# Optimization experiments

Measured on AMD Instinct MI355X. Metric: run time of the kernel, lower is better.

Reference implementation:

```python
import jax, jax.numpy as jnp
import numpy as np

EMBED_DIM = 1024
NUM_HEADS = 16
HEAD_DIM = EMBED_DIM // NUM_HEADS
LN_EPS = 1e-5


def setup_inputs() -> dict:
    key = jax.random.key(0)
    ks = jax.random.split(key, 10)
    B, S, D = 1, 4096, EMBED_DIM
    s = 1.0 / np.sqrt(D)
    inp = {
        'input': jax.random.normal(ks[0], (B, S, D), dtype=jnp.float32),
        'Wq': jax.random.normal(ks[1], (D, D), dtype=jnp.float32) * s,
        'bq': jnp.zeros((D,), dtype=jnp.float32),
        'Wk': jax.random.normal(ks[2], (D, D), dtype=jnp.float32) * s,
        'bk': jnp.zeros((D,), dtype=jnp.float32),
        'Wv': jax.random.normal(ks[3], (D, D), dtype=jnp.float32) * s,
        'bv': jnp.zeros((D,), dtype=jnp.float32),
        'Wo': jax.random.normal(ks[4], (D, D), dtype=jnp.float32) * s,
        'bo': jnp.zeros((D,), dtype=jnp.float32),
        'ln_gamma': jnp.ones((D,), dtype=jnp.float32),
        'ln_beta': jnp.zeros((D,), dtype=jnp.float32),
    }
    return inp


def reference(input, Wq, bq, Wk, bk, Wv, bv, Wo, bo, ln_gamma, ln_beta):
    B, S, D = input.shape
    H, Hd = NUM_HEADS, HEAD_DIM
    # projections (torch Linear: x @ W.T + b)
    q = input @ Wq.T + bq
    k = input @ Wk.T + bk
    v = input @ Wv.T + bv
    # [B, H, S, Hd]
    q = q.reshape(B, S, H, Hd).transpose(0, 2, 1, 3)
    k = k.reshape(B, S, H, Hd).transpose(0, 2, 1, 3)
    v = v.reshape(B, S, H, Hd).transpose(0, 2, 1, 3)
    scores = jnp.einsum('bhqd,bhkd->bhqk', q, k) / jnp.sqrt(jnp.float32(Hd))
    causal = jnp.tril(jnp.ones((S, S), dtype=bool))  # [S, S]
    scores = jnp.where(causal[None, None, :, :], scores, -jnp.inf)
    attn = jax.nn.softmax(scores, axis=-1)  # stable (max-subtract) internally
    out = jnp.einsum('bhqk,bhkd->bhqd', attn, v)
    out = out.transpose(0, 2, 1, 3).reshape(B, S, D)
    out = out @ Wo.T + bo
    out = out + input
    # LayerNorm
    mu = jnp.mean(out, axis=-1, keepdims=True)
    var = jnp.var(out, axis=-1, keepdims=True)
    normed = (out - mu) * jax.lax.rsqrt(var + LN_EPS)
    return normed * ln_gamma + ln_beta
```

## Files before the change

### kernel.cpp

```cpp
#include <hip/hip_runtime.h>
#include <hip/hip_bf16.h>

typedef float floatx4 __attribute__((ext_vector_type(4)));
typedef short short8 __attribute__((ext_vector_type(8)));

#define S_LEN 4096
#define D_DIM 1024
#define NHEAD 16
#define SCALE_LOG2 0.1803368801111204f

__device__ __forceinline__ void gload_lds16(const void* g, void* l) {
  __builtin_amdgcn_global_load_lds(
      (const __attribute__((address_space(1))) unsigned int*)g,
      (__attribute__((address_space(3))) unsigned int*)l, 16, 0, 0);
}

__device__ __forceinline__ unsigned short f2bf_bits(float f) {
  __hip_bfloat16 h = __float2bfloat16(f);
  return __builtin_bit_cast(unsigned short, h);
}

__global__ __launch_bounds__(256) void cvt_all(const float* __restrict__ x,
                                               const float* __restrict__ w0,
                                               const float* __restrict__ w1,
                                               const float* __restrict__ w2,
                                               const float* __restrict__ w3,
                                               unsigned short* __restrict__ xo,
                                               unsigned short* __restrict__ o0,
                                               unsigned short* __restrict__ o1,
                                               unsigned short* __restrict__ o2,
                                               unsigned short* __restrict__ o3) {
  const int bid = blockIdx.x;
  const float* in;
  unsigned short* out;
  int i;
  if (bid < 4096) {
    in = x;
    out = xo;
    i = bid * 256 + threadIdx.x;
  } else {
    const int which = (bid - 4096) >> 10;
    in = which == 0 ? w0 : which == 1 ? w1 : which == 2 ? w2 : w3;
    out = which == 0 ? o0 : which == 1 ? o1 : which == 2 ? o2 : o3;
    i = ((bid - 4096) & 1023) * 256 + threadIdx.x;
  }
  float4 v = reinterpret_cast<const float4*>(in)[i];
  ushort4 u;
  u.x = f2bf_bits(v.x);
  u.y = f2bf_bits(v.y);
  u.z = f2bf_bits(v.z);
  u.w = f2bf_bits(v.w);
  reinterpret_cast<ushort4*>(out)[i] = u;
}

__global__ __launch_bounds__(256) void gemm_qkv(const unsigned short* __restrict__ A,
                                                const unsigned short* __restrict__ WqB,
                                                const unsigned short* __restrict__ WkB,
                                                const unsigned short* __restrict__ WvB,
                                                const float* __restrict__ bq,
                                                const float* __restrict__ bk,
                                                const float* __restrict__ bv,
                                                unsigned short* __restrict__ Qo,
                                                unsigned short* __restrict__ Ko,
                                                unsigned short* __restrict__ VTo) {
  __shared__ __align__(16) unsigned short As[128 * 32];
  __shared__ __align__(16) unsigned short Bs[128 * 32];
  const int K = 1024, N = 1024, M = 4096;
  const int tid = threadIdx.x;
  const int wave = tid >> 6, lane = tid & 63;
  const int seg = blockIdx.y >> 3;
  const int m0 = blockIdx.x * 128, n0 = (blockIdx.y & 7) * 128;
  const unsigned short* B = seg == 0 ? WqB : seg == 1 ? WkB : WvB;
  const float* bias = seg == 0 ? bq : seg == 1 ? bk : bv;
  const int wr = wave >> 1, wc = wave & 1;

  floatx4 acc[4][4] = {};
  const unsigned short* Ab = A + (size_t)m0 * K;
  const unsigned short* Bb = B + (size_t)n0 * K;
  const int srow = lane >> 2, scol = (lane & 3) * 8;
  const int aRow = lane & 15, kOff = (lane >> 4) * 8;

  for (int k0 = 0; k0 < K; k0 += 32) {
#pragma unroll
    for (int i = 0; i < 2; ++i) {
      const int c = wave * 2 + i;
      const int row = c * 16 + srow;
      gload_lds16(Ab + (size_t)row * K + k0 + scol, &As[c * 512]);
      gload_lds16(Bb + (size_t)row * K + k0 + scol, &Bs[c * 512]);
    }
    __syncthreads();
    short8 af[4], bfg[4];
#pragma unroll
    for (int f = 0; f < 4; ++f) {
      af[f] = *reinterpret_cast<const short8*>(&As[(wr * 64 + f * 16 + aRow) * 32 + kOff]);
      bfg[f] = *reinterpret_cast<const short8*>(&Bs[(wc * 64 + f * 16 + aRow) * 32 + kOff]);
    }
#pragma unroll
    for (int fm = 0; fm < 4; ++fm)
#pragma unroll
      for (int fn = 0; fn < 4; ++fn)
        acc[fm][fn] =
            __builtin_amdgcn_mfma_f32_16x16x32_bf16(af[fm], bfg[fn], acc[fm][fn], 0, 0, 0);
    __syncthreads();
  }

  const int rb = (lane >> 4) * 4, cl = lane & 15;
  const float osc = seg == 0 ? SCALE_LOG2 : 1.0f;
#pragma unroll
  for (int fm = 0; fm < 4; ++fm)
#pragma unroll
    for (int fn = 0; fn < 4; ++fn)
#pragma unroll
      for (int r = 0; r < 4; ++r) {
        const int row = m0 + wr * 64 + fm * 16 + rb + r;
        const int col = n0 + wc * 64 + fn * 16 + cl;
        const float v = (acc[fm][fn][r] + bias[col]) * osc;
        if (seg == 0)
          Qo[(size_t)row * N + col] = f2bf_bits(v);
        else if (seg == 1)
          Ko[(size_t)row * N + col] = f2bf_bits(v);
        else
          VTo[(size_t)col * M + row] = f2bf_bits(v);
      }
}

__global__ __launch_bounds__(256) void gemm_o(const unsigned short* __restrict__ A,
                                              const unsigned short* __restrict__ B,
                                              const float* __restrict__ bias,
                                              const float* __restrict__ resid,
                                              float* __restrict__ C) {
  __shared__ __align__(16) unsigned short As[64 * 32];
  __shared__ __align__(16) unsigned short Bs[128 * 32];
  const int K = 1024, N = 1024;
  const int tid = threadIdx.x;
  const int wave = tid >> 6, lane = tid & 63;
  const int m0 = blockIdx.x * 64, n0 = blockIdx.y * 128;
  const int wr = wave >> 1, wc = wave & 1;

  floatx4 acc[2][4] = {};
  const unsigned short* Ab = A + (size_t)m0 * K;
  const unsigned short* Bb = B + (size_t)n0 * K;
  const int srow = lane >> 2, scol = (lane & 3) * 8;
  const int aRow = lane & 15, kOff = (lane >> 4) * 8;

  for (int k0 = 0; k0 < K; k0 += 32) {
#pragma unroll
    for (int i = 0; i < 3; ++i) {
      const int ci = wave * 3 + i;
      if (ci < 4) {
        const int row = ci * 16 + srow;
        gload_lds16(Ab + (size_t)row * K + k0 + scol, &As[ci * 512]);
      } else {
        const int row = (ci - 4) * 16 + srow;
        gload_lds16(Bb + (size_t)row * K + k0 + scol, &Bs[(ci - 4) * 512]);
      }
    }
    __syncthreads();
    short8 af[2], bfg[4];
#pragma unroll
    for (int f = 0; f < 2; ++f)
      af[f] = *reinterpret_cast<const short8*>(&As[(wr * 32 + f * 16 + aRow) * 32 + kOff]);
#pragma unroll
    for (int f = 0; f < 4; ++f)
      bfg[f] = *reinterpret_cast<const short8*>(&Bs[(wc * 64 + f * 16 + aRow) * 32 + kOff]);
#pragma unroll
    for (int fm = 0; fm < 2; ++fm)
#pragma unroll
      for (int fn = 0; fn < 4; ++fn)
        acc[fm][fn] =
            __builtin_amdgcn_mfma_f32_16x16x32_bf16(af[fm], bfg[fn], acc[fm][fn], 0, 0, 0);
    __syncthreads();
  }

  const int rb = (lane >> 4) * 4, cl = lane & 15;
#pragma unroll
  for (int fm = 0; fm < 2; ++fm)
#pragma unroll
    for (int fn = 0; fn < 4; ++fn)
#pragma unroll
      for (int r = 0; r < 4; ++r) {
        const int row = m0 + wr * 32 + fm * 16 + rb + r;
        const int col = n0 + wc * 64 + fn * 16 + cl;
        C[(size_t)row * N + col] =
            acc[fm][fn][r] + bias[col] + resid[(size_t)row * N + col];
      }
}

__global__ __launch_bounds__(256) void attn_fwd(const unsigned short* __restrict__ Q,
                                                const unsigned short* __restrict__ Kg,
                                                const unsigned short* __restrict__ VT,
                                                unsigned short* __restrict__ O) {
  __shared__ __align__(16) unsigned short Ks[2 * 64 * 64];
  __shared__ __align__(16) unsigned short Vs[2 * 64 * 64];
  __shared__ __align__(16) unsigned short Ps[4][16 * 64];

  const int bid = blockIdx.x;
  const int h = bid & 15;
  const int qt = 63 - (bid >> 4);
  const int q0 = qt * 64;
  const int wave = threadIdx.x >> 6, lane = threadIdx.x & 63;
  const int l15 = lane & 15, l4 = lane >> 4;
  const int q7 = l15 & 7;

  const int qrow = q0 + wave * 16 + l15;
  short8 qf[2];
#pragma unroll
  for (int ks = 0; ks < 2; ++ks)
    qf[ks] = *reinterpret_cast<const short8*>(
        &Q[(size_t)qrow * D_DIM + h * 64 + ks * 32 + l4 * 8]);

  floatx4 acco[4] = {};
  float l_run = 0.f;

  auto stageK = [&](int buf, int t) {
    const int kv0 = t * 64;
#pragma unroll
    for (int i = 0; i < 2; ++i) {
      const int seg = wave * 2 + i;
      const int c = seg * 64 + lane;
      const int r = c >> 3, jj = c & 7;
      const int sj = (jj ^ (r & 7)) * 8;
      gload_lds16(&Kg[(size_t)(kv0 + r) * D_DIM + h * 64 + sj],
                  &Ks[buf * 4096 + seg * 512]);
    }
  };
  auto stageV = [&](int buf, int t) {
    const int kv0 = t * 64;
#pragma unroll
    for (int i = 0; i < 2; ++i) {
      const int seg = wave * 2 + i;
      const int c = seg * 64 + lane;
      const int r = c >> 3, jj = c & 7;
      const int sj = (jj ^ (r & 7)) * 8;
      gload_lds16(&VT[(size_t)(h * 64 + r) * S_LEN + kv0 + sj],
                  &Vs[buf * 4096 + seg * 512]);
    }
  };

  const int ntiles = qt + 1;
  stageK(0, 0);

  for (int t = 0; t < ntiles; ++t) {
    asm volatile("s_waitcnt vmcnt(0)" ::: "memory");
    __builtin_amdgcn_s_barrier();
    if (t + 1 < ntiles) stageK((t + 1) & 1, t + 1);
    stageV(t & 1, t);

    const unsigned short* ksb = &Ks[(t & 1) * 4096];

    floatx4 accs[4] = {};
#pragma unroll
    for (int ks = 0; ks < 2; ++ks)
#pragma unroll
      for (int fn = 0; fn < 4; ++fn) {
        const int R = fn * 16 + l15;
        const int J = ks * 4 + l4;
        const short8 kf =
            *reinterpret_cast<const short8*>(&ksb[R * 64 + ((J ^ (R & 7)) * 8)]);
        accs[fn] =
            __builtin_amdgcn_mfma_f32_16x16x32_bf16(kf, qf[ks], accs[fn], 0, 0, 0);
      }

    if (t > 0) {
      const unsigned short* vsb = &Vs[((t - 1) & 1) * 4096];
#pragma unroll
      for (int kh = 0; kh < 2; ++kh) {
        const short8 pf = *reinterpret_cast<const short8*>(
            &Ps[wave][l15 * 64 + (((kh * 4 + l4) ^ q7) << 3)]);
#pragma unroll
        for (int fn = 0; fn < 4; ++fn) {
          const int R = fn * 16 + l15;
          const int J = kh * 4 + l4;
          const short8 vf =
              *reinterpret_cast<const short8*>(&vsb[R * 64 + ((J ^ (R & 7)) * 8)]);
          acco[fn] = __builtin_amdgcn_mfma_f32_16x16x32_bf16(vf, pf, acco[fn], 0, 0, 0);
        }
      }
    }

    const int kv0 = t * 64;
    float p[4][4];
    if (t == ntiles - 1) {
#pragma unroll
      for (int fn = 0; fn < 4; ++fn)
#pragma unroll
        for (int r = 0; r < 4; ++r) {
          const int ka = kv0 + fn * 16 + l4 * 4 + r;
          const float s = (ka > qrow) ? -1e30f : accs[fn][r];
          p[fn][r] = __builtin_amdgcn_exp2f(s);
        }
    } else {
#pragma unroll
      for (int fn = 0; fn < 4; ++fn)
#pragma unroll
        for (int r = 0; r < 4; ++r) p[fn][r] = __builtin_amdgcn_exp2f(accs[fn][r]);
    }
    float rs = 0.f;
#pragma unroll
    for (int fn = 0; fn < 4; ++fn)
#pragma unroll
      for (int r = 0; r < 4; ++r) rs += p[fn][r];
    l_run += rs;

#pragma unroll
    for (int fn = 0; fn < 4; ++fn) {
      const int c = 2 * fn + (l4 >> 1);
      const int off = ((c ^ q7) << 3) + ((l4 & 1) << 2);
      uint2 w;
      w.x = (unsigned)f2bf_bits(p[fn][0]) | ((unsigned)f2bf_bits(p[fn][1]) << 16);
      w.y = (unsigned)f2bf_bits(p[fn][2]) | ((unsigned)f2bf_bits(p[fn][3]) << 16);
      *reinterpret_cast<uint2*>(&Ps[wave][l15 * 64 + off]) = w;
    }
  }

  asm volatile("s_waitcnt vmcnt(0)" ::: "memory");
  __builtin_amdgcn_s_barrier();
  {
    const unsigned short* vsb = &Vs[((ntiles - 1) & 1) * 4096];
#pragma unroll
    for (int kh = 0; kh < 2; ++kh) {
      const short8 pf = *reinterpret_cast<const short8*>(
          &Ps[wave][l15 * 64 + (((kh * 4 + l4) ^ q7) << 3)]);
#pragma unroll
      for (int fn = 0; fn < 4; ++fn) {
        const int R = fn * 16 + l15;
        const int J = kh * 4 + l4;
        const short8 vf =
            *reinterpret_cast<const short8*>(&vsb[R * 64 + ((J ^ (R & 7)) * 8)]);
        acco[fn] = __builtin_amdgcn_mfma_f32_16x16x32_bf16(vf, pf, acco[fn], 0, 0, 0);
      }
    }
  }

  l_run += __shfl_xor(l_run, 16);
  l_run += __shfl_xor(l_run, 32);
  const float inv = 1.f / l_run;
#pragma unroll
  for (int fn = 0; fn < 4; ++fn)
#pragma unroll
    for (int rp = 0; rp < 2; ++rp) {
      const unsigned lo = f2bf_bits(acco[fn][2 * rp] * inv);
      const unsigned hi = f2bf_bits(acco[fn][2 * rp + 1] * inv);
      *reinterpret_cast<unsigned*>(
          &O[(size_t)qrow * D_DIM + h * 64 + fn * 16 + l4 * 4 + rp * 2]) =
          lo | (hi << 16);
    }
}

__global__ __launch_bounds__(256) void ln_kernel(const float* __restrict__ X,
                                                 const float* __restrict__ g,
                                                 const float* __restrict__ b,
                                                 float* __restrict__ Y) {
  const int row = blockIdx.x;
  const int t = threadIdx.x;
  const float4 xv = reinterpret_cast<const float4*>(X + (size_t)row * 1024)[t];
  float s = xv.x + xv.y + xv.z + xv.w;
  float s2 = xv.x * xv.x + xv.y * xv.y + xv.z * xv.z + xv.w * xv.w;
#pragma unroll
  for (int off = 1; off < 64; off <<= 1) {
    s += __shfl_xor(s, off);
    s2 += __shfl_xor(s2, off);
  }
  __shared__ float sr[4], sr2[4];
  const int wave = t >> 6, lane = t & 63;
  if (lane == 0) {
    sr[wave] = s;
    sr2[wave] = s2;
  }
  __syncthreads();
  const float S = sr[0] + sr[1] + sr[2] + sr[3];
  const float S2 = sr2[0] + sr2[1] + sr2[2] + sr2[3];
  const float mu = S * (1.f / 1024.f);
  const float var = S2 * (1.f / 1024.f) - mu * mu;
  const float rstd = rsqrtf(var + 1e-5f);
  const float4 gv = reinterpret_cast<const float4*>(g)[t];
  const float4 bv = reinterpret_cast<const float4*>(b)[t];
  float4 y;
  y.x = (xv.x - mu) * rstd * gv.x + bv.x;
  y.y = (xv.y - mu) * rstd * gv.y + bv.y;
  y.z = (xv.z - mu) * rstd * gv.z + bv.z;
  y.w = (xv.w - mu) * rstd * gv.w + bv.w;
  reinterpret_cast<float4*>(Y + (size_t)row * 1024)[t] = y;
}

extern "C" void kernel_launch(void* const* d_in, const int* in_sizes, int n_in,
                              void* d_out, int out_size, void* d_ws, size_t ws_size,
                              hipStream_t stream) {
  const float* x = (const float*)d_in[0];
  const float* Wq = (const float*)d_in[1];
  const float* bq = (const float*)d_in[2];
  const float* Wk = (const float*)d_in[3];
  const float* bk = (const float*)d_in[4];
  const float* Wv = (const float*)d_in[5];
  const float* bv = (const float*)d_in[6];
  const float* Wo = (const float*)d_in[7];
  const float* bo = (const float*)d_in[8];
  const float* gamma = (const float*)d_in[9];
  const float* beta = (const float*)d_in[10];

  char* ws = (char*)d_ws;
  const size_t MB = (size_t)1 << 20;
  unsigned short* Xb = (unsigned short*)(ws + 0);
  unsigned short* Wqb = (unsigned short*)(ws + 8 * MB);
  unsigned short* Wkb = (unsigned short*)(ws + 10 * MB);
  unsigned short* Wvb = (unsigned short*)(ws + 12 * MB);
  unsigned short* Wob = (unsigned short*)(ws + 16 * MB);
  unsigned short* Qb = (unsigned short*)(ws + 18 * MB);
  unsigned short* Kb = (unsigned short*)(ws + 26 * MB);
  unsigned short* VTb = (unsigned short*)(ws + 34 * MB);
  unsigned short* Ab = (unsigned short*)(ws + 42 * MB);
  float* proj = (float*)(ws + 0);

  cvt_all<<<8192, 256, 0, stream>>>(x, Wq, Wk, Wv, Wo, Xb, Wqb, Wkb, Wvb, Wob);

  gemm_qkv<<<dim3(32, 24), 256, 0, stream>>>(Xb, Wqb, Wkb, Wvb, bq, bk, bv, Qb, Kb,
                                             VTb);

  attn_fwd<<<dim3(1024), 256, 0, stream>>>(Qb, Kb, VTb, Ab);

  gemm_o<<<dim3(64, 8), 256, 0, stream>>>(Ab, Wob, bo, x, proj);

  ln_kernel<<<4096, 256, 0, stream>>>(proj, gamma, beta, (float*)d_out);
}
```

Measured before the change: 142.8 us.

## Double-buffer LDS tiles in QKV and output projection GEMMs

Both projection GEMMs now use two LDS buffers. The global-to-LDS loads for the next K-slice are issued right after the barrier, so they overlap with the MFMA work on the current slice, and the trailing barrier is removed, leaving one barrier per iteration. The cost is twice the shared memory per block, which may lower occupancy. The s_waitcnt vmcnt(0) at the top of each iteration still waits on the prefetch issued in the previous iteration, so the overlap only spans one compute phase.

```diff
diff --git a/kernel.cpp b/kernel.cpp
--- a/kernel.cpp
+++ b/kernel.cpp
@@ -63,8 +63,8 @@
                                                 unsigned short* __restrict__ Qo,
                                                 unsigned short* __restrict__ Ko,
                                                 unsigned short* __restrict__ VTo) {
-  __shared__ __align__(16) unsigned short As[128 * 32];
-  __shared__ __align__(16) unsigned short Bs[128 * 32];
+  __shared__ __align__(16) unsigned short As[2][128 * 32];
+  __shared__ __align__(16) unsigned short Bs[2][128 * 32];
   const int K = 1024, N = 1024, M = 4096;
   const int tid = threadIdx.x;
   const int wave = tid >> 6, lane = tid & 63;
@@ -80,20 +80,29 @@
   const int srow = lane >> 2, scol = (lane & 3) * 8;
   const int aRow = lane & 15, kOff = (lane >> 4) * 8;
 
-  for (int k0 = 0; k0 < K; k0 += 32) {
+  auto stage = [&](int buf, int k0) {
 #pragma unroll
     for (int i = 0; i < 2; ++i) {
       const int c = wave * 2 + i;
       const int row = c * 16 + srow;
-      gload_lds16(Ab + (size_t)row * K + k0 + scol, &As[c * 512]);
-      gload_lds16(Bb + (size_t)row * K + k0 + scol, &Bs[c * 512]);
-    }
-    __syncthreads();
+      gload_lds16(Ab + (size_t)row * K + k0 + scol, &As[buf][c * 512]);
+      gload_lds16(Bb + (size_t)row * K + k0 + scol, &Bs[buf][c * 512]);
+    }
+  };
+
+  stage(0, 0);
+  int buf = 0;
+  for (int k0 = 0; k0 < K; k0 += 32, buf ^= 1) {
+    asm volatile("s_waitcnt vmcnt(0)" ::: "memory");
+    __builtin_amdgcn_s_barrier();
+    if (k0 + 32 < K) stage(buf ^ 1, k0 + 32);
     short8 af[4], bfg[4];
 #pragma unroll
     for (int f = 0; f < 4; ++f) {
-      af[f] = *reinterpret_cast<const short8*>(&As[(wr * 64 + f * 16 + aRow) * 32 + kOff]);
-      bfg[f] = *reinterpret_cast<const short8*>(&Bs[(wc * 64 + f * 16 + aRow) * 32 + kOff]);
+      af[f] =
+          *reinterpret_cast<const short8*>(&As[buf][(wr * 64 + f * 16 + aRow) * 32 + kOff]);
+      bfg[f] =
+          *reinterpret_cast<const short8*>(&Bs[buf][(wc * 64 + f * 16 + aRow) * 32 + kOff]);
     }
 #pragma unroll
     for (int fm = 0; fm < 4; ++fm)
@@ -101,7 +110,6 @@
       for (int fn = 0; fn < 4; ++fn)
         acc[fm][fn] =
             __builtin_amdgcn_mfma_f32_16x16x32_bf16(af[fm], bfg[fn], acc[fm][fn], 0, 0, 0);
-    __syncthreads();
   }
 
   const int rb = (lane >> 4) * 4, cl = lane & 15;
@@ -129,8 +137,8 @@
                                               const float* __restrict__ bias,
                                               const float* __restrict__ resid,
                                               float* __restrict__ C) {
-  __shared__ __align__(16) unsigned short As[64 * 32];
-  __shared__ __align__(16) unsigned short Bs[128 * 32];
+  __shared__ __align__(16) unsigned short As[2][64 * 32];
+  __shared__ __align__(16) unsigned short Bs[2][128 * 32];
   const int K = 1024, N = 1024;
   const int tid = threadIdx.x;
   const int wave = tid >> 6, lane = tid & 63;
@@ -143,33 +151,41 @@
   const int srow = lane >> 2, scol = (lane & 3) * 8;
   const int aRow = lane & 15, kOff = (lane >> 4) * 8;
 
-  for (int k0 = 0; k0 < K; k0 += 32) {
+  auto stage = [&](int buf, int k0) {
 #pragma unroll
     for (int i = 0; i < 3; ++i) {
       const int ci = wave * 3 + i;
       if (ci < 4) {
         const int row = ci * 16 + srow;
-        gload_lds16(Ab + (size_t)row * K + k0 + scol, &As[ci * 512]);
+        gload_lds16(Ab + (size_t)row * K + k0 + scol, &As[buf][ci * 512]);
       } else {
         const int row = (ci - 4) * 16 + srow;
-        gload_lds16(Bb + (size_t)row * K + k0 + scol, &Bs[(ci - 4) * 512]);
-      }
-    }
-    __syncthreads();
+        gload_lds16(Bb + (size_t)row * K + k0 + scol, &Bs[buf][(ci - 4) * 512]);
+      }
+    }
+  };
+
+  stage(0, 0);
+  int buf = 0;
+  for (int k0 = 0; k0 < K; k0 += 32, buf ^= 1) {
+    asm volatile("s_waitcnt vmcnt(0)" ::: "memory");
+    __builtin_amdgcn_s_barrier();
+    if (k0 + 32 < K) stage(buf ^ 1, k0 + 32);
     short8 af[2], bfg[4];
 #pragma unroll
     for (int f = 0; f < 2; ++f)
-      af[f] = *reinterpret_cast<const short8*>(&As[(wr * 32 + f * 16 + aRow) * 32 + kOff]);
+      af[f] =
+          *reinterpret_cast<const short8*>(&As[buf][(wr * 32 + f * 16 + aRow) * 32 + kOff]);
 #pragma unroll
     for (int f = 0; f < 4; ++f)
-      bfg[f] = *reinterpret_cast<const short8*>(&Bs[(wc * 64 + f * 16 + aRow) * 32 + kOff]);
+      bfg[f] =
+          *reinterpret_cast<const short8*>(&Bs[buf][(wc * 64 + f * 16 + aRow) * 32 + kOff]);
 #pragma unroll
     for (int fm = 0; fm < 2; ++fm)
 #pragma unroll
       for (int fn = 0; fn < 4; ++fn)
         acc[fm][fn] =
             __builtin_amdgcn_mfma_f32_16x16x32_bf16(af[fm], bfg[fn], acc[fm][fn], 0, 0, 0);
-    __syncthreads();
   }
 
   const int rb = (lane >> 4) * 4, cl = lane & 15;
```

Result: no change. 143.5 us (median of 2 runs) (+0.5%).
